# Kernel optimization log

Measured on AMD Instinct MI355X. Metric: run time of the kernel, lower is better.

The kernel has to match this reference:

```python
import jax, jax.numpy as jnp
import numpy as np

B, S, D_IN, D_OUT = 4, 2048, 1024, 1024
N_TREES, DEPTH, N_HEADS = 12, 3, 3
N_INTERNAL = 2 ** DEPTH - 1  # 7
N_LEAVES = 2 ** DEPTH        # 8
TEMPERATURE = 1.0
SOFTPLUS_SHIFT = 0.5413      # softplus(0.5413) ~= 1.0, so init node temp ~ 1


def _build_path_indices(depth):
    """Root-to-leaf internal-node indices and go-left directions per leaf."""
    L = 2 ** depth
    pi = np.zeros((L, depth), np.int32)
    pd = np.zeros((L, depth), np.float32)
    for leaf in range(L):
        node = 0
        for d in range(depth):
            pi[leaf, d] = node
            bit = (leaf >> (depth - 1 - d)) & 1
            pd[leaf, d] = 1.0 - bit
            node = 2 * node + 1 + bit
    return pi, pd


def setup_inputs() -> dict:
    key = jax.random.key(0)
    ks = jax.random.split(key, 4)
    x = jax.random.normal(ks[0], (B, S, D_IN), dtype=jnp.float32)
    # normal(0, 0.1) routing init
    decision_weights = 0.1 * jax.random.normal(ks[1], (N_TREES, N_INTERNAL, D_IN), dtype=jnp.float32)
    decision_biases = jnp.zeros((N_TREES, N_INTERNAL), dtype=jnp.float32)
    node_temperature_logits = jnp.zeros((N_TREES, N_INTERNAL), dtype=jnp.float32)
    # nn.Linear default init ~ U(-1/sqrt(D), 1/sqrt(D)); use matching-scale normal
    gate_w = jax.random.normal(ks[2], (N_TREES, D_IN), dtype=jnp.float32) / np.sqrt(D_IN)
    gate_b = jnp.zeros((N_TREES,), dtype=jnp.float32)
    # xavier_normal over each [n_leaves, output_dim] slice
    xav_std = np.sqrt(2.0 / (N_LEAVES + D_OUT))
    leaf_outputs = xav_std * jax.random.normal(ks[3], (N_HEADS, N_TREES, N_LEAVES, D_OUT), dtype=jnp.float32)
    pi, pd = _build_path_indices(DEPTH)
    return {
        "x": x,
        "decision_weights": decision_weights,
        "decision_biases": decision_biases,
        "node_temperature_logits": node_temperature_logits,
        "gate_w": gate_w,
        "gate_b": gate_b,
        "leaf_outputs": leaf_outputs,
        "path_indices": jnp.asarray(pi),
        "path_dirs": jnp.asarray(pd),
    }


def reference(x, decision_weights, decision_biases, node_temperature_logits,
              gate_w, gate_b, leaf_outputs, path_indices, path_dirs):
    # decisions: [B, S, T, N_internal]
    decisions = jnp.einsum('bsd,tnd->bstn', x, decision_weights) + decision_biases
    node_temps = TEMPERATURE * jax.nn.softplus(node_temperature_logits + SOFTPLUS_SHIFT)
    decisions = jax.nn.sigmoid(decisions / node_temps)
    # gather nodes along each root->leaf path: [B, S, T, L, depth]
    relevant = decisions[..., path_indices]
    probs_per_level = path_dirs * relevant + (1.0 - path_dirs) * (1.0 - relevant)
    leaf_probs = probs_per_level.prod(axis=-1)  # [B, S, T, L]
    # softmax gate over trees: [B, S, T]
    weights = jax.nn.softmax(jnp.einsum('bsd,td->bst', x, gate_w) + gate_b, axis=-1)
    # fold tree gate into leaf probs, then contract leaves against leaf outputs
    routed = leaf_probs * weights[..., None]            # [B, S, T, L]
    out = jnp.einsum('bstl,htld->hbsd', routed, leaf_outputs)  # [H, B, S, Dout]
    return out
```

## Files before the change

### kernel.cpp

```cpp
#include <hip/hip_runtime.h>

typedef __attribute__((ext_vector_type(8))) short short8;
typedef __attribute__((ext_vector_type(4))) float floatx4;
typedef unsigned int uint;
typedef unsigned short ushort;
typedef __attribute__((ext_vector_type(4))) uint uintx4;

#define NTOK   8192
#define DIN    1024
#define DOUT   1024
#define NJ     96
#define TOKPB  16
#define DSTR   97
#define SSTR   85
#define RSTR   104
#define LOT_H  (DOUT * NJ)

static __device__ inline ushort f2b(float f) {
    uint u = __builtin_bit_cast(uint, f);
    u = u + 0x7fffu + ((u >> 16) & 1u);
    return (ushort)(u >> 16);
}
static __device__ inline uint pack2(float a, float b) {
    return (uint)f2b(a) | ((uint)f2b(b) << 16);
}

__global__ __launch_bounds__(256) void k_prep(const float* __restrict__ lo,
                                              const float* __restrict__ dw,
                                              const float* __restrict__ gw,
                                              ushort* __restrict__ lot,
                                              ushort* __restrict__ wcat) {
    int i = blockIdx.x * 256 + threadIdx.x;
    if (i < 3 * LOT_H) {
        int h = i / LOT_H;
        int rem = i - h * LOT_H;
        int k = rem >> 10;
        int d = rem & 1023;
        lot[h * LOT_H + d * NJ + k] = f2b(lo[i]);
    } else {
        int j = i - 3 * LOT_H;
        int r = j >> 10, c = j & 1023;
        float v = (r < 84) ? dw[r * DIN + c] : gw[(r - 84) * DIN + c];
        wcat[j] = f2b(v);
    }
}

__global__ __launch_bounds__(512, 4) void k_fused(
    const float* __restrict__ x,
    const ushort* __restrict__ wcat,
    const float* __restrict__ db,
    const float* __restrict__ ntl,
    const float* __restrict__ gb,
    const int*   __restrict__ pi,
    const float* __restrict__ pd,
    const ushort* __restrict__ lot,
    float* __restrict__ out)
{
    __shared__ float decis[TOKPB * DSTR];
    __shared__ float sdecs[TOKPB * SSTR];
    __shared__ __attribute__((aligned(16))) ushort rt[TOKPB][RSTR];
    __shared__ float invt[84];
    __shared__ float biasf[96];
    __shared__ int   pis[24];
    __shared__ float pds[24];

    const int tid = threadIdx.x;
    const int tb  = blockIdx.x * TOKPB;

    if (tid < 84) {
        float z = ntl[tid] + 0.5413f;
        float sp = (z > 20.0f) ? z : log1pf(__expf(z));
        invt[tid]  = 1.0f / sp;
        biasf[tid] = db[tid];
    } else if (tid < 96) {
        biasf[tid] = gb[tid - 84];
    } else if (tid < 120) {
        pis[tid - 96] = pi[tid - 96];
    } else if (tid < 144) {
        pds[tid - 120] = pd[tid - 120];
    }

    const int wave = tid >> 6, lane = tid & 63;
    const int lrow = lane & 15, quad = lane >> 4;

    floatx4 acc0 = (floatx4)(0.0f);
    const int ntc = (wave < 6) ? wave : 0;
    const float*  xr = x    + (size_t)(tb + lrow) * DIN + quad * 8;
    const ushort* w0 = wcat + (size_t)(ntc * 16 + lrow) * DIN + quad * 8;

    if (wave < 6) {
#pragma unroll
        for (int kc = 0; kc < 8; ++kc) {
            short8 a[4];
#pragma unroll
            for (int kt = 0; kt < 4; ++kt) {
                floatx4 u = *(const floatx4*)(xr + kc * 128 + kt * 32);
                floatx4 v = *(const floatx4*)(xr + kc * 128 + kt * 32 + 4);
                union { short8 s; uint w[4]; } pk;
                pk.w[0] = pack2(u[0], u[1]);
                pk.w[1] = pack2(u[2], u[3]);
                pk.w[2] = pack2(v[0], v[1]);
                pk.w[3] = pack2(v[2], v[3]);
                a[kt] = pk.s;
            }
#pragma unroll
            for (int kt = 0; kt < 4; ++kt) {
                short8 b0 = *(const short8*)(w0 + kc * 128 + kt * 32);
                acc0 = __builtin_amdgcn_mfma_f32_16x16x32_bf16(a[kt], b0, acc0, 0, 0, 0);
            }
        }
    }

    short8 bb[3][6];
#define LOADB(B, G) do { \
    _Pragma("unroll") for (int q_ = 0; q_ < 2; ++q_) { \
        int c_ = wave * 384 + ((G) * 2 + q_) * 16; \
        int h_ = c_ >> 10; \
        int d_ = (c_ & 1023) + lrow; \
        const ushort* bp_ = lot + (size_t)h_ * LOT_H + (size_t)d_ * NJ + quad * 8; \
        _Pragma("unroll") for (int kk_ = 0; kk_ < 3; ++kk_) \
            bb[B][q_ * 3 + kk_] = *(const short8*)(bp_ + kk_ * 32); \
    } } while (0)

    LOADB(0, 0);
    LOADB(1, 1);

    if (wave < 6) {
#pragma unroll
        for (int r = 0; r < 4; ++r)
            decis[(quad * 4 + r) * DSTR + wave * 16 + lrow] = acc0[r];
    }
    __syncthreads();

#pragma unroll
    for (int i = 0; i < 3; ++i) {
        int idx = tid + 512 * i;
        if (idx < TOKPB * 84) {
            int tk = idx / 84, nd = idx - tk * 84;
            float dv = (decis[tk * DSTR + nd] + biasf[nd]) * invt[nd];
            sdecs[tk * SSTR + nd] = 1.0f / (1.0f + __expf(-dv));
        }
    }
    __syncthreads();

    {
        const int tk = tid >> 5, l = (tid >> 2) & 7, th = tid & 3;
        float g[12], gm = -1e30f;
#pragma unroll
        for (int tt = 0; tt < 12; ++tt) {
            g[tt] = decis[tk * DSTR + 84 + tt] + biasf[84 + tt];
            gm = fmaxf(gm, g[tt]);
        }
        float gs = 0.0f;
#pragma unroll
        for (int tt = 0; tt < 12; ++tt) { g[tt] = __expf(g[tt] - gm); gs += g[tt]; }
        float ginv = 1.0f / gs;

        const int   n0 = pis[l * 3 + 0], n1 = pis[l * 3 + 1], n2 = pis[l * 3 + 2];
        const float d0 = pds[l * 3 + 0], d1 = pds[l * 3 + 1], d2 = pds[l * 3 + 2];
        const float* sd = sdecs + tk * SSTR;
        const int t0 = th * 3;
#pragma unroll
        for (int t = 0; t < 3; ++t) {
            int tt = t0 + t;
            float s0 = sd[tt * 7 + n0], s1 = sd[tt * 7 + n1], s2 = sd[tt * 7 + n2];
            float pb = g[tt] * ginv
                     * (d0 * s0 + (1.0f - d0) * (1.0f - s0))
                     * (d1 * s1 + (1.0f - d1) * (1.0f - s1))
                     * (d2 * s2 + (1.0f - d2) * (1.0f - s2));
            rt[tk][tt * 8 + l] = f2b(pb);
        }
    }
    __syncthreads();

    {
        short8 a[3];
#pragma unroll
        for (int kk = 0; kk < 3; ++kk)
            a[kk] = *(const short8*)(&rt[lrow][quad * 8 + kk * 32]);

#pragma unroll
        for (int g = 0; g < 12; ++g) {
            const int cur = g % 3;
            if (g < 10) LOADB((g + 2) % 3, g + 2);
#pragma unroll
            for (int q = 0; q < 2; ++q) {
                floatx4 c0 = (floatx4)(0.0f);
#pragma unroll
                for (int kk = 0; kk < 3; ++kk)
                    c0 = __builtin_amdgcn_mfma_f32_16x16x32_bf16(a[kk], bb[cur][q * 3 + kk], c0, 0, 0, 0);
                int c = wave * 384 + (g * 2 + q) * 16;
                int h = c >> 10;
                int d = (c & 1023) + lrow;
                float* ob = out + ((size_t)h * NTOK + tb) * DOUT + d;
#pragma unroll
                for (int r = 0; r < 4; ++r)
                    __builtin_nontemporal_store(c0[r], ob + (size_t)(quad * 4 + r) * DOUT);
            }
        }
#undef LOADB
    }
}

extern "C" void kernel_launch(void* const* d_in, const int* in_sizes, int n_in,
                              void* d_out, int out_size, void* d_ws, size_t ws_size,
                              hipStream_t stream) {
    const float* x   = (const float*)d_in[0];
    const float* dw  = (const float*)d_in[1];
    const float* db  = (const float*)d_in[2];
    const float* ntl = (const float*)d_in[3];
    const float* gw  = (const float*)d_in[4];
    const float* gb  = (const float*)d_in[5];
    const float* lo  = (const float*)d_in[6];
    const int*   pi  = (const int*)d_in[7];
    const float* pd  = (const float*)d_in[8];
    float* out = (float*)d_out;

    ushort* lot  = (ushort*)d_ws;
    ushort* wcat = lot + (size_t)3 * LOT_H;

    k_prep<<<dim3((3 * LOT_H + NJ * DIN) / 256), dim3(256), 0, stream>>>(lo, dw, gw, lot, wcat);
    k_fused<<<dim3(NTOK / TOKPB), dim3(512), 0, stream>>>(x, wcat, db, ntl, gb, pi, pd, lot, out);
}
```

Measured before the change: 178.3 us.

## Stage leaf-contraction outputs through LDS for coalesced 16-byte global stores

The output phase now computes four 16x16 MFMA tiles per step (64 columns) and writes them to a per-wave LDS staging buffer. Each lane then issues float4 stores covering contiguous 128-byte row segments, replacing scattered scalar nontemporal stores. The triple-buffered register prefetch of leaf weights is dropped in favour of loads issued inside the loop. This adds about 36 KB of LDS, which may lower occupancy, and exposes more load latency.

```diff
diff --git a/kernel.cpp b/kernel.cpp
--- a/kernel.cpp
+++ b/kernel.cpp
@@ -14,6 +14,7 @@
 #define DSTR   97
 #define SSTR   85
 #define RSTR   104
+#define STG    72
 #define LOT_H  (DOUT * NJ)
 
 static __device__ inline ushort f2b(float f) {
@@ -59,6 +60,7 @@
     __shared__ float decis[TOKPB * DSTR];
     __shared__ float sdecs[TOKPB * SSTR];
     __shared__ __attribute__((aligned(16))) ushort rt[TOKPB][RSTR];
+    __shared__ __attribute__((aligned(16))) float stg[8][TOKPB * STG];
     __shared__ float invt[84];
     __shared__ float biasf[96];
     __shared__ int   pis[24];
@@ -111,20 +113,6 @@
         }
     }
 
-    short8 bb[3][6];
-#define LOADB(B, G) do { \
-    _Pragma("unroll") for (int q_ = 0; q_ < 2; ++q_) { \
-        int c_ = wave * 384 + ((G) * 2 + q_) * 16; \
-        int h_ = c_ >> 10; \
-        int d_ = (c_ & 1023) + lrow; \
-        const ushort* bp_ = lot + (size_t)h_ * LOT_H + (size_t)d_ * NJ + quad * 8; \
-        _Pragma("unroll") for (int kk_ = 0; kk_ < 3; ++kk_) \
-            bb[B][q_ * 3 + kk_] = *(const short8*)(bp_ + kk_ * 32); \
-    } } while (0)
-
-    LOADB(0, 0);
-    LOADB(1, 1);
-
     if (wave < 6) {
 #pragma unroll
         for (int r = 0; r < 4; ++r)
@@ -179,26 +167,45 @@
         for (int kk = 0; kk < 3; ++kk)
             a[kk] = *(const short8*)(&rt[lrow][quad * 8 + kk * 32]);
 
-#pragma unroll
-        for (int g = 0; g < 12; ++g) {
-            const int cur = g % 3;
-            if (g < 10) LOADB((g + 2) % 3, g + 2);
-#pragma unroll
-            for (int q = 0; q < 2; ++q) {
-                floatx4 c0 = (floatx4)(0.0f);
-#pragma unroll
-                for (int kk = 0; kk < 3; ++kk)
-                    c0 = __builtin_amdgcn_mfma_f32_16x16x32_bf16(a[kk], bb[cur][q * 3 + kk], c0, 0, 0, 0);
-                int c = wave * 384 + (g * 2 + q) * 16;
-                int h = c >> 10;
-                int d = (c & 1023) + lrow;
-                float* ob = out + ((size_t)h * NTOK + tb) * DOUT + d;
-#pragma unroll
-                for (int r = 0; r < 4; ++r)
-                    __builtin_nontemporal_store(c0[r], ob + (size_t)(quad * 4 + r) * DOUT);
-            }
-        }
-#undef LOADB
+        float* wb = &stg[wave][0];
+
+#pragma unroll
+        for (int g = 0; g < 6; ++g) {
+            const int s    = wave * 384 + g * 64;
+            const int h    = s >> 10;
+            const int dcol = s & 1023;
+            const ushort* bp0 = lot + (size_t)h * LOT_H
+                              + (size_t)(dcol + lrow) * NJ + quad * 8;
+
+            floatx4 c0 = (floatx4)(0.0f), c1 = (floatx4)(0.0f);
+            floatx4 c2 = (floatx4)(0.0f), c3 = (floatx4)(0.0f);
+#pragma unroll
+            for (int kk = 0; kk < 3; ++kk) {
+                short8 b0 = *(const short8*)(bp0 + 0 * 16 * NJ + kk * 32);
+                short8 b1 = *(const short8*)(bp0 + 1 * 16 * NJ + kk * 32);
+                short8 b2 = *(const short8*)(bp0 + 2 * 16 * NJ + kk * 32);
+                short8 b3 = *(const short8*)(bp0 + 3 * 16 * NJ + kk * 32);
+                c0 = __builtin_amdgcn_mfma_f32_16x16x32_bf16(a[kk], b0, c0, 0, 0, 0);
+                c1 = __builtin_amdgcn_mfma_f32_16x16x32_bf16(a[kk], b1, c1, 0, 0, 0);
+                c2 = __builtin_amdgcn_mfma_f32_16x16x32_bf16(a[kk], b2, c2, 0, 0, 0);
+                c3 = __builtin_amdgcn_mfma_f32_16x16x32_bf16(a[kk], b3, c3, 0, 0, 0);
+            }
+#pragma unroll
+            for (int r = 0; r < 4; ++r) {
+                wb[(quad * 4 + r) * STG +  0 + lrow] = c0[r];
+                wb[(quad * 4 + r) * STG + 16 + lrow] = c1[r];
+                wb[(quad * 4 + r) * STG + 32 + lrow] = c2[r];
+                wb[(quad * 4 + r) * STG + 48 + lrow] = c3[r];
+            }
+#pragma unroll
+            for (int i = 0; i < 4; ++i) {
+                const int row  = (i & 1) * 8 + (lane >> 3);
+                const int colh = (i >> 1) * 32 + (lane & 7) * 4;
+                floatx4 v = *(const floatx4*)(wb + row * STG + colh);
+                *(floatx4*)(out + ((size_t)h * NTOK + tb + row) * DOUT
+                            + dcol + colh) = v;
+            }
+        }
     }
 }
 
```

Measured after the change: 177.9 us. Within noise of the previous version (-0.2%).
